# Kernel optimization log

Measured on AMD Instinct MI355X. Metric: run time of the kernel, lower is better.

The kernel has to match this reference:

```python
import jax, jax.numpy as jnp
import numpy as np

HEADS = 8
DIM_HEAD = 32
IH = IW = 32
EPS = 1e-5


def _relative_index(ih, iw):
    # faithful reproduction of the torch buffer computation
    coords = np.stack(np.meshgrid(np.arange(ih), np.arange(iw), indexing='ij')).reshape(2, -1)  # (2, n)
    rel = coords[:, :, None] - coords[:, None, :]  # (2, n, n)
    rel[0] += ih - 1
    rel[1] += iw - 1
    rel[0] *= 2 * iw - 1
    return rel.transpose(1, 2, 0).sum(-1).reshape(-1).astype(np.int32)  # (n*n,)


def setup_inputs() -> dict:
    key = jax.random.key(0)
    ks = jax.random.split(key, 8)
    C, HID = 256, 1024
    s = 0.02
    inp = {
        'x': jax.random.normal(ks[0], (16, C, IH, IW), jnp.float32),
        'qkv_w': jax.random.normal(ks[1], (C, 3 * HEADS * DIM_HEAD), jnp.float32) * s,
        'proj_w': jax.random.normal(ks[2], (HEADS * DIM_HEAD, C), jnp.float32) * s,
        'proj_b': jnp.zeros((C,), jnp.float32),
        'ffn_w1': jax.random.normal(ks[3], (C, HID), jnp.float32) * s,
        'ffn_b1': jnp.zeros((HID,), jnp.float32),
        'ffn_w2': jax.random.normal(ks[4], (HID, C), jnp.float32) * s,
        'ffn_b2': jnp.zeros((C,), jnp.float32),
        'norm1_w': jnp.ones((C,), jnp.float32),
        'norm1_b': jnp.zeros((C,), jnp.float32),
        'norm2_w': jnp.ones((C,), jnp.float32),
        'norm2_b': jnp.zeros((C,), jnp.float32),
        'bias_table': jax.random.normal(ks[5], ((2 * IH - 1) * (2 * IW - 1), HEADS), jnp.float32) * s,
        'rel_index': jnp.asarray(_relative_index(IH, IW)),
    }
    return inp


def _layernorm(x, w, b):
    mu = jnp.mean(x, -1, keepdims=True)
    var = jnp.mean(jnp.square(x - mu), -1, keepdims=True)
    return (x - mu) * jax.lax.rsqrt(var + EPS) * w + b


def reference(x, qkv_w, proj_w, proj_b, ffn_w1, ffn_b1, ffn_w2, ffn_b2,
              norm1_w, norm1_b, norm2_w, norm2_b, bias_table, rel_index):
    B, C, H, W = x.shape
    n = H * W
    scale = DIM_HEAD ** -0.5

    # b c h w -> b n c
    xt = x.reshape(B, C, n).transpose(0, 2, 1)
    x1 = _layernorm(xt, norm1_w, norm1_b)

    qkv = x1 @ qkv_w  # (B, n, 3*inner)
    q, k, v = jnp.split(qkv, 3, axis=-1)
    def heads(t):
        return t.reshape(B, n, HEADS, DIM_HEAD).transpose(0, 2, 1, 3)  # b h n d
    q, k, v = heads(q), heads(k), heads(v)

    dots = jnp.einsum('bhid,bhjd->bhij', q, k) * scale
    # gathered relative position bias: (n*n, heads) -> (1, heads, n, n)
    bias = bias_table[rel_index].reshape(n, n, HEADS).transpose(2, 0, 1)[None]
    attn = jax.nn.softmax(dots + bias, axis=-1)
    out = jnp.einsum('bhij,bhjd->bhid', attn, v)  # b h n d
    out = out.transpose(0, 2, 1, 3).reshape(B, n, HEADS * DIM_HEAD)
    out = out @ proj_w + proj_b  # (B, n, C)

    # back to b c h w and first residual
    x1 = out.transpose(0, 2, 1).reshape(B, C, H, W)
    x3 = x1 + x

    # FFN branch
    x4 = x3.reshape(B, C, n).transpose(0, 2, 1)
    x4 = _layernorm(x4, norm2_w, norm2_b)
    x4 = jax.nn.gelu(x4 @ ffn_w1 + ffn_b1, approximate=False) @ ffn_w2 + ffn_b2
    x4 = x4.transpose(0, 2, 1).reshape(B, C, H, W)
    return x3 + x4
```

## Files before the change

kernel.cpp:

```cpp
#include <hip/hip_runtime.h>
#include <math.h>

#define BATCH 16
#define CH    256
#define NT    1024
#define NH    8
#define DH    32
#define HID   1024
#define MROWS (BATCH * NT)
#define LN_EPS 1e-5f

typedef unsigned short u16;
typedef unsigned int u32;
typedef __attribute__((ext_vector_type(8))) short short8;
typedef __attribute__((ext_vector_type(4))) short short4v;
typedef __attribute__((ext_vector_type(4))) float f32x4;

struct __align__(8) US4 { u16 x, y, z, w; };
struct __align__(16) F4 { float x, y, z, w; };

#define MFMA(a, b, c) __builtin_amdgcn_mfma_f32_16x16x32_bf16((a), (b), (c), 0, 0, 0)
#define MFMA16(a, b, c) __builtin_amdgcn_mfma_f32_16x16x16bf16_1k((a), (b), (c), 0, 0, 0)

#define LOG2E 1.4426950408889634f
#define QSCALE (0.17677669529663687f * 1.4426950408889634f)

__device__ __forceinline__ float bf2f(u16 u) {
  union { unsigned int i; float f; } v; v.i = ((unsigned int)u) << 16; return v.f;
}
__device__ __forceinline__ u16 f2bf(float f) {
  union { float f; unsigned int i; } v; v.f = f;
  unsigned int i = v.i;
  return (u16)((i + 0x7fffu + ((i >> 16) & 1u)) >> 16);
}
__device__ __forceinline__ u32 pack_bf16_pair(float lo, float hi) {
  union { float f; u32 i; } a, b; a.f = lo; b.f = hi;
#if defined(__HIP_DEVICE_COMPILE__)
  return __builtin_amdgcn_perm(b.i, a.i, 0x07060302u);
#else
  return (b.i & 0xFFFF0000u) | (a.i >> 16);
#endif
}
__device__ __forceinline__ float fast_exp2(float x) {
#if defined(__HIP_DEVICE_COMPILE__)
  return __builtin_amdgcn_exp2f(x);
#else
  return exp2f(x);
#endif
}
__device__ __forceinline__ float fast_gelu(float x) {
  const float c = 2.0f * LOG2E * 0.7978845608028654f;
  float t = fast_exp2(c * (x + 0.044715f * x * x * x));
  return x * t / (t + 1.0f);
}
__device__ __forceinline__ void llds16(const u16* g, u16* l) {
  __builtin_amdgcn_global_load_lds(
      (const __attribute__((address_space(1))) u32*)g,
      (__attribute__((address_space(3))) u32*)l, 16, 0, 0);
}

__global__ __launch_bounds__(256) void k_transpose(const float* __restrict__ in,
                                                   u16* __restrict__ out,
                                                   int K, int N) {
  __shared__ u16 tl[64][66];
  const int t = threadIdx.x;
  const int kb = blockIdx.x * 64, nb = blockIdx.y * 64;
#pragma unroll
  for (int it = 0; it < 16; ++it) {
    int n_l = t & 63, k_l = it * 4 + (t >> 6);
    tl[k_l][n_l] = f2bf(in[(size_t)(kb + k_l) * N + nb + n_l]);
  }
  __syncthreads();
#pragma unroll
  for (int it = 0; it < 16; ++it) {
    int k_l = t & 63, n_l = it * 4 + (t >> 6);
    out[(size_t)(nb + n_l) * K + kb + k_l] = tl[k_l][n_l];
  }
}

__global__ __launch_bounds__(256) void k_prep_bias(const float* __restrict__ table,
                                                   const int* __restrict__ rel,
                                                   u16* __restrict__ biasL) {
  const int t = threadIdx.x;
  const int jt = blockIdx.x & 31, isl = blockIdx.x >> 5;
  const int jp = t & 31, io = t >> 5;
  for (int ib = isl * 128; ib < isl * 128 + 128; ib += 8) {
    int i = ib + io;
    int idx = rel[(size_t)i * NT + jt * 32 + jp];
#pragma unroll
    for (int h = 0; h < NH; ++h) {
      biasL[(((size_t)h * 32 + jt) * 1024 + i) * 32 + jp] =
          f2bf(table[(size_t)idx * NH + h] * LOG2E);
    }
  }
}

__global__ __launch_bounds__(256) void k_ln1(const float* __restrict__ x,
                                             const float* __restrict__ w,
                                             const float* __restrict__ b,
                                             u16* __restrict__ x1) {
  __shared__ u16 tile[CH][68];
  __shared__ float red_s[4][64], red_q[4][64], mu_s[64], rs_s[64];
  const int t = threadIdx.x;
  const int bb = blockIdx.x >> 4, pb = blockIdx.x & 15;
  const int pos0 = pb * 64;
#pragma unroll
  for (int it = 0; it < 16; ++it) {
    int c = it * 16 + (t >> 4), p4 = (t & 15) * 4;
    F4 v = *(const F4*)(x + ((size_t)bb * CH + c) * NT + pos0 + p4);
    US4 o; o.x = f2bf(v.x); o.y = f2bf(v.y); o.z = f2bf(v.z); o.w = f2bf(v.w);
    *(US4*)&tile[c][p4] = o;
  }
  __syncthreads();
  {
    int pos = t & 63, g = t >> 6;
    float s = 0.f, q = 0.f;
#pragma unroll 8
    for (int cc = 0; cc < 64; ++cc) {
      float v = bf2f(tile[g * 64 + cc][pos]);
      s += v; q += v * v;
    }
    red_s[g][pos] = s; red_q[g][pos] = q;
  }
  __syncthreads();
  if (t < 64) {
    float s = red_s[0][t] + red_s[1][t] + red_s[2][t] + red_s[3][t];
    float q = red_q[0][t] + red_q[1][t] + red_q[2][t] + red_q[3][t];
    float mu = s * (1.f / CH);
    float var = q * (1.f / CH) - mu * mu;
    mu_s[t] = mu;
    rs_s[t] = rsqrtf(fmaxf(var, 0.f) + LN_EPS);
  }
  __syncthreads();
  {
    const int c = t;
    const float wv = w[c], bv = b[c];
    for (int pos = 0; pos < 64; ++pos) {
      float v = (bf2f(tile[c][pos]) - mu_s[pos]) * rs_s[pos] * wv + bv;
      x1[((size_t)bb * NT + pos0 + pos) * CH + c] = f2bf(v);
    }
  }
}

template <int K>
__device__ __forceinline__ void gemm128(const u16* __restrict__ A,
                                        const u16* __restrict__ Bt,
                                        int r0, int c0, int tid,
                                        u16* lA, u16* lB,
                                        f32x4 acc[4][4]) {
  const int wave = tid >> 6, lane = tid & 63;
  const int wm = (wave >> 1) * 64, wn = (wave & 1) * 64;
  const int l16 = lane & 15, quad = lane >> 4;
  const int srow = lane >> 2;
  const int scol = (lane & 3) * 8;
  const u16* gA0 = A + (size_t)(r0 + wave * 16 + srow) * K + scol;
  const u16* gA1 = A + (size_t)(r0 + wave * 16 + 64 + srow) * K + scol;
  const u16* gB0 = Bt + (size_t)(c0 + wave * 16 + srow) * K + scol;
  const u16* gB1 = Bt + (size_t)(c0 + wave * 16 + 64 + srow) * K + scol;
  u16* lA0 = lA + (wave * 16) * 32;
  u16* lA1 = lA + (wave * 16 + 64) * 32;
  u16* lB0 = lB + (wave * 16) * 32;
  u16* lB1 = lB + (wave * 16 + 64) * 32;
  for (int k0 = 0; k0 < K; k0 += 32) {
    __syncthreads();
    llds16(gA0 + k0, lA0);
    llds16(gA1 + k0, lA1);
    llds16(gB0 + k0, lB0);
    llds16(gB1 + k0, lB1);
    __syncthreads();
    short8 af[4], bf[4];
#pragma unroll
    for (int i = 0; i < 4; ++i)
      af[i] = *(const short8*)&lA[(wm + i * 16 + l16) * 32 + quad * 8];
#pragma unroll
    for (int j = 0; j < 4; ++j)
      bf[j] = *(const short8*)&lB[(wn + j * 16 + l16) * 32 + quad * 8];
#pragma unroll
    for (int i = 0; i < 4; ++i)
#pragma unroll
      for (int j = 0; j < 4; ++j)
        acc[i][j] = MFMA(af[i], bf[j], acc[i][j]);
  }
}

#define GEMM_PROLOGUE(KVAL, APTR, BPTR)                                  \
  __shared__ __align__(16) u16 lA[128 * 32];                             \
  __shared__ __align__(16) u16 lB[128 * 32];                             \
  const int tid = threadIdx.x;                                           \
  const int wave = tid >> 6, lane = tid & 63;                            \
  const int wm = (wave >> 1) * 64, wn = (wave & 1) * 64;                 \
  const int l16 = lane & 15, quad = lane >> 4;                           \
  const int r0 = blockIdx.x * 128, c0 = blockIdx.y * 128;                \
  f32x4 acc[4][4];                                                       \
  _Pragma("unroll") for (int i = 0; i < 4; ++i)                          \
  _Pragma("unroll") for (int j = 0; j < 4; ++j) acc[i][j] = 0.f;         \
  gemm128<KVAL>(APTR, BPTR, r0, c0, tid, lA, lB, acc);

__global__ __launch_bounds__(256) void k_gemm_qkv(const u16* __restrict__ x1,
                                                  const u16* __restrict__ wT,
                                                  u16* __restrict__ q,
                                                  u16* __restrict__ k,
                                                  u16* __restrict__ vT) {
  GEMM_PROLOGUE(CH, x1, wT)
#pragma unroll
  for (int j = 0; j < 4; ++j) {
    int col = c0 + wn + j * 16 + l16;
    int which = col >> 8, rem = col & 255, h = rem >> 5, dd = rem & 31;
#pragma unroll
    for (int i = 0; i < 4; ++i) {
      int row0 = r0 + wm + i * 16 + quad * 4;
      int bb = row0 >> 10, pos = row0 & 1023;
      if (which == 2) {
        US4 o;
        o.x = f2bf(acc[i][j][0]); o.y = f2bf(acc[i][j][1]);
        o.z = f2bf(acc[i][j][2]); o.w = f2bf(acc[i][j][3]);
        *(US4*)(vT + (((size_t)bb * NH + h) * DH + dd) * NT + pos) = o;
      } else {
        u16* dst = (which == 0) ? q : k;
        float mul = (which == 0) ? QSCALE : 1.0f;
#pragma unroll
        for (int r = 0; r < 4; ++r)
          dst[(((size_t)bb * NH + h) * NT + pos + r) * DH + dd] =
              f2bf(acc[i][j][r] * mul);
      }
    }
  }
}

__global__ __launch_bounds__(256) void k_gemm_proj(const u16* __restrict__ ao,
                                                   const u16* __restrict__ wT,
                                                   const float* __restrict__ pb,
                                                   const float* __restrict__ x,
                                                   u16* __restrict__ x3) {
  GEMM_PROLOGUE(CH, ao, wT)
#pragma unroll
  for (int j = 0; j < 4; ++j) {
    int col = c0 + wn + j * 16 + l16;
    float bias = pb[col];
#pragma unroll
    for (int i = 0; i < 4; ++i) {
      int row0 = r0 + wm + i * 16 + quad * 4;
      int bb = row0 >> 10, pos = row0 & 1023;
#pragma unroll
      for (int r = 0; r < 4; ++r) {
        float val = acc[i][j][r] + bias + x[((size_t)bb * CH + col) * NT + pos + r];
        x3[(size_t)(row0 + r) * CH + col] = f2bf(val);
      }
    }
  }
}

__global__ __launch_bounds__(256) void k_gemm_ffn1(const u16* __restrict__ a,
                                                   const u16* __restrict__ wT,
                                                   const float* __restrict__ b1,
                                                   u16* __restrict__ hmat) {
  GEMM_PROLOGUE(CH, a, wT)
#pragma unroll
  for (int j = 0; j < 4; ++j) {
    int col = c0 + wn + j * 16 + l16;
    float bias = b1[col];
#pragma unroll
    for (int i = 0; i < 4; ++i) {
      int row0 = r0 + wm + i * 16 + quad * 4;
#pragma unroll
      for (int r = 0; r < 4; ++r) {
        float v = acc[i][j][r] + bias;
        hmat[(size_t)(row0 + r) * HID + col] = f2bf(fast_gelu(v));
      }
    }
  }
}

__global__ __launch_bounds__(256) void k_gemm_ffn2(const u16* __restrict__ a,
                                                   const u16* __restrict__ wT,
                                                   const float* __restrict__ b2,
                                                   u16* __restrict__ x4) {
  GEMM_PROLOGUE(HID, a, wT)
#pragma unroll
  for (int j = 0; j < 4; ++j) {
    int col = c0 + wn + j * 16 + l16;
    float bias = b2[col];
#pragma unroll
    for (int i = 0; i < 4; ++i) {
      int row0 = r0 + wm + i * 16 + quad * 4;
#pragma unroll
      for (int r = 0; r < 4; ++r)
        x4[(size_t)(row0 + r) * CH + col] = f2bf(acc[i][j][r] + bias);
    }
  }
}

__global__ __launch_bounds__(256) void k_attn(const u16* __restrict__ q,
                                              const u16* __restrict__ k,
                                              const u16* __restrict__ vT,
                                              const u16* __restrict__ biasL,
                                              u16* __restrict__ ao) {
  __shared__ u16 Ks[256][40];
  __shared__ u16 Vt[32][264];
  const int tid = threadIdx.x;
  const int wave = tid >> 6, lane = tid & 63;
  const int quad = lane >> 4, l16 = lane & 15;
  const int bh = blockIdx.x >> 4, qt = blockIdx.x & 15;
  const int h = bh & 7, bb = bh >> 3;
  const int i0 = qt * 64 + wave * 16;

  short8 aq = *(const short8*)(q + ((size_t)bh * NT + i0 + l16) * DH + quad * 8);
  const u16* bias_base =
      biasL + (((size_t)h * 32) * 1024 + (i0 + l16)) * 32 + quad * 4;

  float l_loc = 0.f;
  f32x4 accd0 = 0.f, accd1 = 0.f;

  for (int chunk = 0; chunk < 4; ++chunk) {
    __syncthreads();
    const int rbase = chunk * 256;
    {
      const int srow = tid >> 3, sdd = (tid & 7) * 4;
#pragma unroll
      for (int it = 0; it < 8; ++it) {
        int rl = it * 32 + srow;
        US4 kv = *(const US4*)(k + ((size_t)bh * NT + rbase + rl) * DH + sdd);
        *(US4*)&Ks[rl][sdd] = kv;
      }
      const int j4 = (tid & 63) * 4;
#pragma unroll
      for (int it = 0; it < 8; ++it) {
        int d = it * 4 + wave;
        US4 vv = *(const US4*)(vT + ((size_t)bh * DH + d) * NT + rbase + j4);
        *(US4*)&Vt[d][j4] = vv;
      }
    }
    __syncthreads();

#pragma unroll 2
    for (int j0 = 0; j0 < 256; j0 += 32) {
      const int jt = (rbase + j0) >> 5;
      const u16* bl = bias_base + (size_t)jt * 32768;
      US4 b0 = *(const US4*)bl;
      US4 b1 = *(const US4*)(bl + 16);
      f32x4 cc0, cc1;
      cc0[0] = bf2f(b0.x); cc0[1] = bf2f(b0.y);
      cc0[2] = bf2f(b0.z); cc0[3] = bf2f(b0.w);
      cc1[0] = bf2f(b1.x); cc1[1] = bf2f(b1.y);
      cc1[2] = bf2f(b1.z); cc1[3] = bf2f(b1.w);
      short8 ak0 = *(const short8*)&Ks[j0 + l16][quad * 8];
      short8 ak1 = *(const short8*)&Ks[j0 + 16 + l16][quad * 8];
      f32x4 s0 = MFMA(ak0, aq, cc0);
      f32x4 s1 = MFMA(ak1, aq, cc1);
      float p00 = fast_exp2(s0[0]), p01 = fast_exp2(s0[1]);
      float p02 = fast_exp2(s0[2]), p03 = fast_exp2(s0[3]);
      float p10 = fast_exp2(s1[0]), p11 = fast_exp2(s1[1]);
      float p12 = fast_exp2(s1[2]), p13 = fast_exp2(s1[3]);
      l_loc += ((p00 + p01) + (p02 + p03)) + ((p10 + p11) + (p12 + p13));
      union { u32 u[2]; short4v s; } pa0, pa1;
      pa0.u[0] = pack_bf16_pair(p00, p01);
      pa0.u[1] = pack_bf16_pair(p02, p03);
      pa1.u[0] = pack_bf16_pair(p10, p11);
      pa1.u[1] = pack_bf16_pair(p12, p13);
      short4v vb00 = *(const short4v*)&Vt[l16][j0 + quad * 4];
      short4v vb10 = *(const short4v*)&Vt[l16][j0 + 16 + quad * 4];
      short4v vb01 = *(const short4v*)&Vt[16 + l16][j0 + quad * 4];
      short4v vb11 = *(const short4v*)&Vt[16 + l16][j0 + 16 + quad * 4];
      accd0 = MFMA16(pa0.s, vb00, accd0);
      accd1 = MFMA16(pa0.s, vb01, accd1);
      accd0 = MFMA16(pa1.s, vb10, accd0);
      accd1 = MFMA16(pa1.s, vb11, accd1);
    }
  }
  l_loc += __shfl_xor(l_loc, 16);
  l_loc += __shfl_xor(l_loc, 32);
#pragma unroll
  for (int r = 0; r < 4; ++r) {
    float lr = __shfl(l_loc, quad * 4 + r);
    float inv = 1.0f / lr;
    int row = i0 + quad * 4 + r;
    u16* o = ao + ((size_t)bb * NT + row) * CH + h * DH;
    o[l16]      = f2bf(accd0[r] * inv);
    o[16 + l16] = f2bf(accd1[r] * inv);
  }
}

__global__ __launch_bounds__(256) void k_ln2(const u16* __restrict__ x3,
                                             const float* __restrict__ w,
                                             const float* __restrict__ b,
                                             u16* __restrict__ x4ln) {
  const int wave = threadIdx.x >> 6, lane = threadIdx.x & 63;
  const size_t row = (size_t)blockIdx.x * 4 + wave;
  US4 u = *(const US4*)(x3 + row * CH + lane * 4);
  float v0 = bf2f(u.x), v1 = bf2f(u.y), v2 = bf2f(u.z), v3 = bf2f(u.w);
  float s = v0 + v1 + v2 + v3;
  float qq = v0 * v0 + v1 * v1 + v2 * v2 + v3 * v3;
#pragma unroll
  for (int mask = 1; mask <= 32; mask <<= 1) {
    s += __shfl_xor(s, mask);
    qq += __shfl_xor(qq, mask);
  }
  float mu = s * (1.f / CH);
  float var = qq * (1.f / CH) - mu * mu;
  float rs = rsqrtf(fmaxf(var, 0.f) + LN_EPS);
  F4 uw = *(const F4*)(w + lane * 4);
  F4 ub = *(const F4*)(b + lane * 4);
  US4 o;
  o.x = f2bf((v0 - mu) * rs * uw.x + ub.x);
  o.y = f2bf((v1 - mu) * rs * uw.y + ub.y);
  o.z = f2bf((v2 - mu) * rs * uw.z + ub.z);
  o.w = f2bf((v3 - mu) * rs * uw.w + ub.w);
  *(US4*)(x4ln + row * CH + lane * 4) = o;
}

__global__ __launch_bounds__(256) void k_add_t(const u16* __restrict__ x3,
                                               const u16* __restrict__ x4,
                                               float* __restrict__ out) {
  __shared__ float tl[64][66];
  const int t = threadIdx.x;
  const int bb = blockIdx.x >> 6;
  const int pb = (blockIdx.x >> 2) & 15, cb = blockIdx.x & 3;
  const int pos0 = pb * 64, c0 = cb * 64;
#pragma unroll
  for (int it = 0; it < 16; ++it) {
    int c_l = t & 63, p_l = it * 4 + (t >> 6);
    size_t ro = ((size_t)bb * NT + pos0 + p_l) * CH + c0 + c_l;
    tl[p_l][c_l] = bf2f(x3[ro]) + bf2f(x4[ro]);
  }
  __syncthreads();
#pragma unroll
  for (int it = 0; it < 16; ++it) {
    int p_l = t & 63, c_l = it * 4 + (t >> 6);
    out[((size_t)bb * CH + c0 + c_l) * NT + pos0 + p_l] = tl[p_l][c_l];
  }
}

extern "C" void kernel_launch(void* const* d_in, const int* in_sizes, int n_in,
                              void* d_out, int out_size, void* d_ws, size_t ws_size,
                              hipStream_t stream) {
  const float* x       = (const float*)d_in[0];
  const float* qkv_w   = (const float*)d_in[1];
  const float* proj_w  = (const float*)d_in[2];
  const float* proj_b  = (const float*)d_in[3];
  const float* ffn_w1  = (const float*)d_in[4];
  const float* ffn_b1  = (const float*)d_in[5];
  const float* ffn_w2  = (const float*)d_in[6];
  const float* ffn_b2  = (const float*)d_in[7];
  const float* norm1_w = (const float*)d_in[8];
  const float* norm1_b = (const float*)d_in[9];
  const float* norm2_w = (const float*)d_in[10];
  const float* norm2_b = (const float*)d_in[11];
  const float* btab    = (const float*)d_in[12];
  const int* rel       = (const int*)d_in[13];
  float* out = (float*)d_out;

  char* ws = (char*)d_ws;
  size_t off = 0;
  auto alloc = [&](size_t bytes) { char* p = ws + off; off += bytes; return p; };
  u16* qkv_wT  = (u16*)alloc((size_t)768 * 256 * 2);
  u16* proj_wT = (u16*)alloc((size_t)256 * 256 * 2);
  u16* w1T     = (u16*)alloc((size_t)1024 * 256 * 2);
  u16* w2T     = (u16*)alloc((size_t)256 * 1024 * 2);
  u16* biasL   = (u16*)alloc((size_t)NH * NT * NT * 2);
  u16* qm      = (u16*)alloc((size_t)MROWS * CH * 2);
  u16* km      = (u16*)alloc((size_t)MROWS * CH * 2);
  u16* vm      = (u16*)alloc((size_t)MROWS * CH * 2);
  u16* bufX    = (u16*)alloc((size_t)MROWS * CH * 2);
  u16* x3      = (u16*)alloc((size_t)MROWS * CH * 2);
  u16* ffn_h = biasL;
  u16* x4ln  = vm;
  u16* x1 = bufX;
  u16* ao = bufX;
  u16* x4 = bufX;
  (void)ws_size; (void)in_sizes; (void)n_in; (void)out_size;

  k_transpose<<<dim3(4, 12), 256, 0, stream>>>(qkv_w, qkv_wT, 256, 768);
  k_transpose<<<dim3(4, 4), 256, 0, stream>>>(proj_w, proj_wT, 256, 256);
  k_transpose<<<dim3(4, 16), 256, 0, stream>>>(ffn_w1, w1T, 256, 1024);
  k_transpose<<<dim3(16, 4), 256, 0, stream>>>(ffn_w2, w2T, 1024, 256);
  k_prep_bias<<<256, 256, 0, stream>>>(btab, rel, biasL);
  k_ln1<<<BATCH * 16, 256, 0, stream>>>(x, norm1_w, norm1_b, x1);
  k_gemm_qkv<<<dim3(MROWS / 128, 6), 256, 0, stream>>>(x1, qkv_wT, qm, km, vm);
  k_attn<<<BATCH * NH * 16, 256, 0, stream>>>(qm, km, vm, biasL, ao);
  k_gemm_proj<<<dim3(MROWS / 128, 2), 256, 0, stream>>>(ao, proj_wT, proj_b, x, x3);
  k_ln2<<<MROWS / 4, 256, 0, stream>>>(x3, norm2_w, norm2_b, x4ln);
  k_gemm_ffn1<<<dim3(MROWS / 128, 8), 256, 0, stream>>>(x4ln, w1T, ffn_b1, ffn_h);
  k_gemm_ffn2<<<dim3(MROWS / 128, 2), 256, 0, stream>>>(ffn_h, w2T, ffn_b2, x4);
  k_add_t<<<BATCH * 16 * 4, 256, 0, stream>>>(x3, x4, out);
}
```

Measured before the change: 253.8 us.

## Fuse residual add into FFN2, add 128x64 GEMM tile, MFMA row-sums, permuted bias

Several changes land together. The final residual add and transpose are fused into the FFN2 epilogue, which writes fp32 output directly in channel-major layout; this removes the separate k_add_t pass and the x4 round trip. A new 128x64 GEMM tile doubles the grid for the proj and FFN2 GEMMs, which have N=256. In attention, the softmax row sums are computed by an extra MFMA against a vector of ones instead of scalar adds and shuffles, and the bias table is permuted so each lane loads 8 bias values in one 16-byte load. The risks are strided epilogue stores in FFN2, more MFMA work in attention, and lower reuse per tile.

```diff
diff --git a/kernel.cpp b/kernel.cpp
--- a/kernel.cpp
+++ b/kernel.cpp
@@ -80,16 +80,17 @@
 
 __global__ __launch_bounds__(256) void k_prep_bias(const float* __restrict__ table,
                                                    const int* __restrict__ rel,
-                                                   u16* __restrict__ biasL) {
+                                                   u16* __restrict__ biasP) {
   const int t = threadIdx.x;
   const int jt = blockIdx.x & 31, isl = blockIdx.x >> 5;
   const int jp = t & 31, io = t >> 5;
+  const int slot = ((jp >> 2) & 3) * 8 + (jp >> 4) * 4 + (jp & 3);
   for (int ib = isl * 128; ib < isl * 128 + 128; ib += 8) {
     int i = ib + io;
     int idx = rel[(size_t)i * NT + jt * 32 + jp];
 #pragma unroll
     for (int h = 0; h < NH; ++h) {
-      biasL[(((size_t)h * 32 + jt) * 1024 + i) * 32 + jp] =
+      biasP[(((size_t)h * 32 + jt) * 1024 + i) * 32 + slot] =
           f2bf(table[(size_t)idx * NH + h] * LOG2E);
     }
   }
@@ -196,6 +197,57 @@
   _Pragma("unroll") for (int j = 0; j < 4; ++j) acc[i][j] = 0.f;         \
   gemm128<KVAL>(APTR, BPTR, r0, c0, tid, lA, lB, acc);
 
+template <int K>
+__device__ __forceinline__ void gemm128x64(const u16* __restrict__ A,
+                                           const u16* __restrict__ Bt,
+                                           int r0, int c0, int tid,
+                                           u16* lA, u16* lB,
+                                           f32x4 acc[2][4]) {
+  const int wave = tid >> 6, lane = tid & 63;
+  const int wm = wave * 32;
+  const int l16 = lane & 15, quad = lane >> 4;
+  const int srow = lane >> 2;
+  const int scol = (lane & 3) * 8;
+  const u16* gA0 = A + (size_t)(r0 + wm + srow) * K + scol;
+  const u16* gA1 = A + (size_t)(r0 + wm + 16 + srow) * K + scol;
+  const u16* gB0 = Bt + (size_t)(c0 + wave * 16 + srow) * K + scol;
+  u16* lA0 = lA + (size_t)wm * 32;
+  u16* lA1 = lA + (size_t)(wm + 16) * 32;
+  u16* lB0 = lB + (size_t)(wave * 16) * 32;
+  for (int k0 = 0; k0 < K; k0 += 32) {
+    __syncthreads();
+    llds16(gA0 + k0, lA0);
+    llds16(gA1 + k0, lA1);
+    llds16(gB0 + k0, lB0);
+    __syncthreads();
+    short8 af[2], bf[4];
+#pragma unroll
+    for (int i = 0; i < 2; ++i)
+      af[i] = *(const short8*)&lA[(wm + i * 16 + l16) * 32 + quad * 8];
+#pragma unroll
+    for (int j = 0; j < 4; ++j)
+      bf[j] = *(const short8*)&lB[(j * 16 + l16) * 32 + quad * 8];
+#pragma unroll
+    for (int i = 0; i < 2; ++i)
+#pragma unroll
+      for (int j = 0; j < 4; ++j)
+        acc[i][j] = MFMA(af[i], bf[j], acc[i][j]);
+  }
+}
+
+#define GEMM_PROLOGUE64(KVAL, APTR, BPTR)                                \
+  __shared__ __align__(16) u16 lA[128 * 32];                             \
+  __shared__ __align__(16) u16 lB[64 * 32];                              \
+  const int tid = threadIdx.x;                                           \
+  const int wave = tid >> 6, lane = tid & 63;                            \
+  const int wm = wave * 32;                                              \
+  const int l16 = lane & 15, quad = lane >> 4;                           \
+  const int r0 = blockIdx.x * 128, c0 = blockIdx.y * 64;                 \
+  f32x4 acc[2][4];                                                       \
+  _Pragma("unroll") for (int i = 0; i < 2; ++i)                          \
+  _Pragma("unroll") for (int j = 0; j < 4; ++j) acc[i][j] = 0.f;         \
+  gemm128x64<KVAL>(APTR, BPTR, r0, c0, tid, lA, lB, acc);
+
 __global__ __launch_bounds__(256) void k_gemm_qkv(const u16* __restrict__ x1,
                                                   const u16* __restrict__ wT,
                                                   u16* __restrict__ q,
@@ -232,13 +284,13 @@
                                                    const float* __restrict__ pb,
                                                    const float* __restrict__ x,
                                                    u16* __restrict__ x3) {
-  GEMM_PROLOGUE(CH, ao, wT)
+  GEMM_PROLOGUE64(CH, ao, wT)
 #pragma unroll
   for (int j = 0; j < 4; ++j) {
-    int col = c0 + wn + j * 16 + l16;
+    int col = c0 + j * 16 + l16;
     float bias = pb[col];
 #pragma unroll
-    for (int i = 0; i < 4; ++i) {
+    for (int i = 0; i < 2; ++i) {
       int row0 = r0 + wm + i * 16 + quad * 4;
       int bb = row0 >> 10, pos = row0 & 1023;
 #pragma unroll
@@ -274,18 +326,23 @@
 __global__ __launch_bounds__(256) void k_gemm_ffn2(const u16* __restrict__ a,
                                                    const u16* __restrict__ wT,
                                                    const float* __restrict__ b2,
-                                                   u16* __restrict__ x4) {
-  GEMM_PROLOGUE(HID, a, wT)
+                                                   const u16* __restrict__ x3,
+                                                   float* __restrict__ out) {
+  GEMM_PROLOGUE64(HID, a, wT)
 #pragma unroll
   for (int j = 0; j < 4; ++j) {
-    int col = c0 + wn + j * 16 + l16;
+    int col = c0 + j * 16 + l16;
     float bias = b2[col];
 #pragma unroll
-    for (int i = 0; i < 4; ++i) {
+    for (int i = 0; i < 2; ++i) {
       int row0 = r0 + wm + i * 16 + quad * 4;
+      int bb = row0 >> 10, pos = row0 & 1023;
+      F4 o;
+      float* po = &o.x;
 #pragma unroll
       for (int r = 0; r < 4; ++r)
-        x4[(size_t)(row0 + r) * CH + col] = f2bf(acc[i][j][r] + bias);
+        po[r] = acc[i][j][r] + bias + bf2f(x3[(size_t)(row0 + r) * CH + col]);
+      *(F4*)(out + ((size_t)bb * CH + col) * NT + pos) = o;
     }
   }
 }
@@ -293,7 +350,7 @@
 __global__ __launch_bounds__(256) void k_attn(const u16* __restrict__ q,
                                               const u16* __restrict__ k,
                                               const u16* __restrict__ vT,
-                                              const u16* __restrict__ biasL,
+                                              const u16* __restrict__ biasP,
                                               u16* __restrict__ ao) {
   __shared__ u16 Ks[256][40];
   __shared__ u16 Vt[32][264];
@@ -306,9 +363,11 @@
 
   short8 aq = *(const short8*)(q + ((size_t)bh * NT + i0 + l16) * DH + quad * 8);
   const u16* bias_base =
-      biasL + (((size_t)h * 32) * 1024 + (i0 + l16)) * 32 + quad * 4;
-
-  float l_loc = 0.f;
+      biasP + (((size_t)h * 32) * 1024 + (i0 + l16)) * 32 + quad * 8;
+
+  short4v vones;
+  vones[0] = vones[1] = vones[2] = vones[3] = (short)0x3F80;
+  f32x4 accl = 0.f;
   f32x4 accd0 = 0.f, accd1 = 0.f;
 
   for (int chunk = 0; chunk < 4; ++chunk) {
@@ -335,14 +394,14 @@
 #pragma unroll 2
     for (int j0 = 0; j0 < 256; j0 += 32) {
       const int jt = (rbase + j0) >> 5;
-      const u16* bl = bias_base + (size_t)jt * 32768;
-      US4 b0 = *(const US4*)bl;
-      US4 b1 = *(const US4*)(bl + 16);
+      short8 be = *(const short8*)(bias_base + (size_t)jt * 32768);
+      const u16* bep = (const u16*)&be;
       f32x4 cc0, cc1;
-      cc0[0] = bf2f(b0.x); cc0[1] = bf2f(b0.y);
-      cc0[2] = bf2f(b0.z); cc0[3] = bf2f(b0.w);
-      cc1[0] = bf2f(b1.x); cc1[1] = bf2f(b1.y);
-      cc1[2] = bf2f(b1.z); cc1[3] = bf2f(b1.w);
+#pragma unroll
+      for (int r = 0; r < 4; ++r) {
+        cc0[r] = bf2f(bep[r]);
+        cc1[r] = bf2f(bep[4 + r]);
+      }
       short8 ak0 = *(const short8*)&Ks[j0 + l16][quad * 8];
       short8 ak1 = *(const short8*)&Ks[j0 + 16 + l16][quad * 8];
       f32x4 s0 = MFMA(ak0, aq, cc0);
@@ -351,7 +410,6 @@
       float p02 = fast_exp2(s0[2]), p03 = fast_exp2(s0[3]);
       float p10 = fast_exp2(s1[0]), p11 = fast_exp2(s1[1]);
       float p12 = fast_exp2(s1[2]), p13 = fast_exp2(s1[3]);
-      l_loc += ((p00 + p01) + (p02 + p03)) + ((p10 + p11) + (p12 + p13));
       union { u32 u[2]; short4v s; } pa0, pa1;
       pa0.u[0] = pack_bf16_pair(p00, p01);
       pa0.u[1] = pack_bf16_pair(p02, p03);
@@ -363,16 +421,15 @@
       short4v vb11 = *(const short4v*)&Vt[16 + l16][j0 + 16 + quad * 4];
       accd0 = MFMA16(pa0.s, vb00, accd0);
       accd1 = MFMA16(pa0.s, vb01, accd1);
+      accl  = MFMA16(pa0.s, vones, accl);
       accd0 = MFMA16(pa1.s, vb10, accd0);
       accd1 = MFMA16(pa1.s, vb11, accd1);
-    }
-  }
-  l_loc += __shfl_xor(l_loc, 16);
-  l_loc += __shfl_xor(l_loc, 32);
+      accl  = MFMA16(pa1.s, vones, accl);
+    }
+  }
 #pragma unroll
   for (int r = 0; r < 4; ++r) {
-    float lr = __shfl(l_loc, quad * 4 + r);
-    float inv = 1.0f / lr;
+    float inv = 1.0f / accl[r];
     int row = i0 + quad * 4 + r;
     u16* o = ao + ((size_t)bb * NT + row) * CH + h * DH;
     o[l16]      = f2bf(accd0[r] * inv);
@@ -406,28 +463,6 @@
   o.z = f2bf((v2 - mu) * rs * uw.z + ub.z);
   o.w = f2bf((v3 - mu) * rs * uw.w + ub.w);
   *(US4*)(x4ln + row * CH + lane * 4) = o;
-}
-
-__global__ __launch_bounds__(256) void k_add_t(const u16* __restrict__ x3,
-                                               const u16* __restrict__ x4,
-                                               float* __restrict__ out) {
-  __shared__ float tl[64][66];
-  const int t = threadIdx.x;
-  const int bb = blockIdx.x >> 6;
-  const int pb = (blockIdx.x >> 2) & 15, cb = blockIdx.x & 3;
-  const int pos0 = pb * 64, c0 = cb * 64;
-#pragma unroll
-  for (int it = 0; it < 16; ++it) {
-    int c_l = t & 63, p_l = it * 4 + (t >> 6);
-    size_t ro = ((size_t)bb * NT + pos0 + p_l) * CH + c0 + c_l;
-    tl[p_l][c_l] = bf2f(x3[ro]) + bf2f(x4[ro]);
-  }
-  __syncthreads();
-#pragma unroll
-  for (int it = 0; it < 16; ++it) {
-    int p_l = t & 63, c_l = it * 4 + (t >> 6);
-    out[((size_t)bb * CH + c0 + c_l) * NT + pos0 + p_l] = tl[p_l][c_l];
-  }
 }
 
 extern "C" void kernel_launch(void* const* d_in, const int* in_sizes, int n_in,
@@ -456,30 +491,28 @@
   u16* proj_wT = (u16*)alloc((size_t)256 * 256 * 2);
   u16* w1T     = (u16*)alloc((size_t)1024 * 256 * 2);
   u16* w2T     = (u16*)alloc((size_t)256 * 1024 * 2);
-  u16* biasL   = (u16*)alloc((size_t)NH * NT * NT * 2);
+  u16* biasP   = (u16*)alloc((size_t)NH * NT * NT * 2);
   u16* qm      = (u16*)alloc((size_t)MROWS * CH * 2);
   u16* km      = (u16*)alloc((size_t)MROWS * CH * 2);
   u16* vm      = (u16*)alloc((size_t)MROWS * CH * 2);
   u16* bufX    = (u16*)alloc((size_t)MROWS * CH * 2);
   u16* x3      = (u16*)alloc((size_t)MROWS * CH * 2);
-  u16* ffn_h = biasL;
+  u16* ffn_h = biasP;
   u16* x4ln  = vm;
   u16* x1 = bufX;
   u16* ao = bufX;
-  u16* x4 = bufX;
   (void)ws_size; (void)in_sizes; (void)n_in; (void)out_size;
 
   k_transpose<<<dim3(4, 12), 256, 0, stream>>>(qkv_w, qkv_wT, 256, 768);
   k_transpose<<<dim3(4, 4), 256, 0, stream>>>(proj_w, proj_wT, 256, 256);
   k_transpose<<<dim3(4, 16), 256, 0, stream>>>(ffn_w1, w1T, 256, 1024);
   k_transpose<<<dim3(16, 4), 256, 0, stream>>>(ffn_w2, w2T, 1024, 256);
-  k_prep_bias<<<256, 256, 0, stream>>>(btab, rel, biasL);
+  k_prep_bias<<<256, 256, 0, stream>>>(btab, rel, biasP);
   k_ln1<<<BATCH * 16, 256, 0, stream>>>(x, norm1_w, norm1_b, x1);
   k_gemm_qkv<<<dim3(MROWS / 128, 6), 256, 0, stream>>>(x1, qkv_wT, qm, km, vm);
-  k_attn<<<BATCH * NH * 16, 256, 0, stream>>>(qm, km, vm, biasL, ao);
-  k_gemm_proj<<<dim3(MROWS / 128, 2), 256, 0, stream>>>(ao, proj_wT, proj_b, x, x3);
+  k_attn<<<BATCH * NH * 16, 256, 0, stream>>>(qm, km, vm, biasP, ao);
+  k_gemm_proj<<<dim3(MROWS / 128, 4), 256, 0, stream>>>(ao, proj_wT, proj_b, x, x3);
   k_ln2<<<MROWS / 4, 256, 0, stream>>>(x3, norm2_w, norm2_b, x4ln);
   k_gemm_ffn1<<<dim3(MROWS / 128, 8), 256, 0, stream>>>(x4ln, w1T, ffn_b1, ffn_h);
-  k_gemm_ffn2<<<dim3(MROWS / 128, 2), 256, 0, stream>>>(ffn_h, w2T, ffn_b2, x4);
-  k_add_t<<<BATCH * 16 * 4, 256, 0, stream>>>(x3, x4, out);
-}
+  k_gemm_ffn2<<<dim3(MROWS / 128, 4), 256, 0, stream>>>(ffn_h, w2T, ffn_b2, x3, out);
+}
```

Measured after the change: 236.3 us. -6.9%, faster.
